# Kernel tuning notes

Hardware: AMD Instinct MI355X
Metric: run time of the kernel (lower is better)

The kernel has to match this reference:

```python
import jax, jax.numpy as jnp
import numpy as np

D_MODEL = 2048
NUM_HEADS = 16
HEAD_DIM = D_MODEL // NUM_HEADS  # 128; scale uses head_dim even though attention is over full d_model
B, S = 2, 2048


def setup_inputs() -> dict:
    key = jax.random.key(0)
    ks = jax.random.split(key, 5)
    x = jax.random.normal(ks[0], (B, S, D_MODEL), dtype=jnp.float32)
    # causal additive mask, as typically passed to this module (2D, sliced mask[-s:, :kv])
    neg = jnp.float32(-1e9)
    mask = jnp.where(jnp.triu(jnp.ones((S, S), dtype=bool), k=1), neg, jnp.float32(0.0))
    std = 1.0 / np.sqrt(D_MODEL)
    Wq = jax.random.normal(ks[1], (D_MODEL, D_MODEL), dtype=jnp.float32) * std
    Wk = jax.random.normal(ks[2], (D_MODEL, D_MODEL), dtype=jnp.float32) * std
    Wv = jax.random.normal(ks[3], (D_MODEL, D_MODEL), dtype=jnp.float32) * std
    Wo = jax.random.normal(ks[4], (D_MODEL, D_MODEL), dtype=jnp.float32) * std
    return {"x": x, "mask": mask, "Wq": Wq, "Wk": Wk, "Wv": Wv, "Wo": Wo}


def reference(x, mask, Wq, Wk, Wv, Wo):
    # nn.Linear(bias=False): y = x @ W^T
    q = jnp.einsum('bsd,ed->bse', x, Wq)  # [B,S,D]
    k = jnp.einsum('bsd,ed->bse', x, Wk)
    v = jnp.einsum('bsd,ed->bse', x, Wv)
    scale = jnp.float32(HEAD_DIM ** -0.5)
    # NOTE: faithful to source — contraction over full d_model, no head split
    scores = jnp.einsum('bsd,btd->bst', q, k) * scale  # [B,S,S]
    scores = scores + mask  # mask[-s:, :kv] == mask here (s == kv)
    weights = jax.nn.softmax(scores, axis=-1)
    out = jnp.einsum('bst,btd->bsd', weights, v)
    return jnp.einsum('bsd,ed->bse', out, Wo)
```

## Files before the change

### kernel.cpp

```cpp
#include <hip/hip_runtime.h>

#define DM  2048
#define SQ  2048
#define NB  2
#define BSZ (NB * SQ)

typedef _Float16 f16x8 __attribute__((ext_vector_type(8)));
typedef __attribute__((ext_vector_type(4))) float f32x4;

#define ASG(p) (const __attribute__((address_space(1))) void*)(p)
#define ASL(p) (__attribute__((address_space(3))) void*)(p)

__device__ __forceinline__ unsigned short f2h(float f) {
  union { _Float16 h; unsigned short u; } x;
  x.h = (_Float16)f;
  return x.u;
}

__global__ __launch_bounds__(256) void cast_f32(const float4* __restrict__ in,
                                                ushort4* __restrict__ out,
                                                int n4) {
  int i = blockIdx.x * 256 + threadIdx.x;
  if (i >= n4) return;
  float4 v = in[i];
  ushort4 h;
  h.x = f2h(v.x); h.y = f2h(v.y); h.z = f2h(v.z); h.w = f2h(v.w);
  out[i] = h;
}

__global__ __launch_bounds__(256) void cast_w4(const float4* __restrict__ a,
                                               const float4* __restrict__ b,
                                               const float4* __restrict__ c,
                                               const float4* __restrict__ d,
                                               ushort4* __restrict__ out,
                                               int n4per) {
  int i = blockIdx.x * 256 + threadIdx.x;
  int seg = i / n4per, j = i - seg * n4per;
  const float4* src = (seg == 0) ? a : (seg == 1) ? b : (seg == 2) ? c : d;
  float4 v = src[j];
  ushort4 h;
  h.x = f2h(v.x); h.y = f2h(v.y); h.z = f2h(v.z); h.w = f2h(v.w);
  out[i] = h;
}

#define SB() __builtin_amdgcn_sched_barrier(0)
#define BARX() do { SB(); __builtin_amdgcn_s_barrier(); SB(); } while (0)

#define STAGE8(BUFL, HALF, T) do { \
    const unsigned short* G_ = ((HALF) < 2) ? Ab : Bb; \
    const int ldG_ = ((HALF) < 2) ? ldA : ldB; \
    const int r0_ = (((HALF) < 2) ? bm0 : bn0) + ((HALF) & 1) * 128; \
    const long k0_ = (long)((T) << 6); \
    char* db_ = ldsb + (BUFL) * 65536 + (HALF) * 16384 + tid * 16; \
    const unsigned short* s0_ = G_ + (long)(r0_ + srow) * ldG_ + k0_ + scsw; \
    const unsigned short* s1_ = G_ + (long)(r0_ + 64 + srow) * ldG_ + k0_ + scsw; \
    __builtin_amdgcn_global_load_lds(ASG(s0_), ASL(db_), 16, 0, 0); \
    __builtin_amdgcn_global_load_lds(ASG(s1_), ASL(db_ + 8192), 16, 0, 0); \
  } while (0)

#define LDA8(BUFL, MQ, Af) do { \
    const char* ba_ = ldsb + (BUFL) * 65536 + wm * 16384 + (MQ) * 8192 + arow; \
    _Pragma("unroll") for (int mm_ = 0; mm_ < 4; mm_++) { \
      Af[mm_][0] = *(const f16x8*)(ba_ + mm_ * 2048 + sl0); \
      Af[mm_][1] = *(const f16x8*)(ba_ + mm_ * 2048 + sl1); } \
  } while (0)

#define LDB8(BUFL, NQ, Bf) do { \
    const char* bb_ = ldsb + (BUFL) * 65536 + 32768 + (wn * 2 + (NQ)) * 4096 + arow; \
    _Pragma("unroll") for (int nn_ = 0; nn_ < 2; nn_++) { \
      Bf[nn_][0] = *(const f16x8*)(bb_ + nn_ * 2048 + sl0); \
      Bf[nn_][1] = *(const f16x8*)(bb_ + nn_ * 2048 + sl1); } \
  } while (0)

#define PH8(Af, Bf, MQ, NQ) do { \
    __builtin_amdgcn_s_setprio(1); \
    _Pragma("unroll") for (int ks_ = 0; ks_ < 2; ks_++) \
    _Pragma("unroll") for (int mm_ = 0; mm_ < 4; mm_++) \
    _Pragma("unroll") for (int nn_ = 0; nn_ < 2; nn_++) \
      acc[(MQ) * 4 + mm_][(NQ) * 2 + nn_] = __builtin_amdgcn_mfma_f32_16x16x32_f16( \
          Af[mm_][ks_], Bf[nn_][ks_], acc[(MQ) * 4 + mm_][(NQ) * 2 + nn_], 0, 0, 0); \
    __builtin_amdgcn_s_setprio(0); \
  } while (0)

#define GROUP8(BUFL, T) do { \
    LDA8(BUFL, 0, a0); LDB8(BUFL, 0, b0); \
    LDA8(BUFL, 1, a1); \
    if ((T) + 1 < NT) STAGE8(BUFL ^ 1, 3, (T) + 1); \
    PH8(a0, b0, 0, 0); \
    BARX(); \
    LDB8(BUFL, 1, b1); \
    PH8(a1, b0, 1, 0); \
    BARX(); \
    if ((T) + 2 < NT) STAGE8(BUFL, 0, (T) + 2); \
    PH8(a1, b1, 1, 1); \
    BARX(); \
    if ((T) + 2 < NT) { STAGE8(BUFL, 1, (T) + 2); STAGE8(BUFL, 2, (T) + 2); } \
    PH8(a0, b1, 0, 1); \
    SB(); \
    if ((T) + 1 < NT) { \
      if ((T) + 1 == NT - 1) { asm volatile("s_waitcnt vmcnt(0)" ::: "memory"); } \
      else                   { asm volatile("s_waitcnt vmcnt(6)" ::: "memory"); } \
    } \
    __builtin_amdgcn_s_barrier(); \
    SB(); \
  } while (0)

template <int OM>
__global__ __launch_bounds__(512, 2) void gemm8p(
    const unsigned short* __restrict__ A, const unsigned short* __restrict__ B,
    float* __restrict__ Cf, unsigned short* __restrict__ Ch,
    int K, int ldA, int ldB, int ldC) {
  __shared__ __align__(16) char ldsarr[131072];
  char* ldsb = ldsarr;

  const int bm0 = blockIdx.x * 256;
  const int bn0 = blockIdx.y * 256;
  const unsigned short* Ab = A;
  const unsigned short* Bb = B;

  const int tid = threadIdx.x, lane = tid & 63, wid = tid >> 6;
  const int wm = wid >> 2, wn = wid & 3;
  const int fr = lane & 15, fq = lane >> 4;
  const int NT = K >> 6;

  const int sl0 = ((fq ^ (fr & 7)) << 4);
  const int sl1 = (((4 + fq) ^ (fr & 7)) << 4);
  const int arow = fr << 7;

  const int srow = tid >> 3;
  const int scsw = ((tid & 7) ^ (srow & 7)) << 3;

  f32x4 acc[8][4];
#pragma unroll
  for (int m = 0; m < 8; m++)
#pragma unroll
    for (int n = 0; n < 4; n++)
#pragma unroll
      for (int r = 0; r < 4; r++) acc[m][n][r] = 0.f;

  f16x8 a0[4][2], a1[4][2], b0[2][2], b1[2][2];

  STAGE8(0, 0, 0); STAGE8(0, 1, 0); STAGE8(0, 2, 0); STAGE8(0, 3, 0);
  STAGE8(1, 0, 1); STAGE8(1, 1, 1); STAGE8(1, 2, 1);
  asm volatile("s_waitcnt vmcnt(6)" ::: "memory");
  __builtin_amdgcn_s_barrier();
  SB();

  for (int t = 0; t < NT; t += 2) {
    GROUP8(0, t);
    GROUP8(1, t + 1);
  }

#pragma unroll
  for (int mq = 0; mq < 2; mq++)
#pragma unroll
    for (int mm = 0; mm < 4; mm++)
#pragma unroll
      for (int nq = 0; nq < 2; nq++)
#pragma unroll
        for (int nn = 0; nn < 2; nn++) {
          const int col = bn0 + wn * 64 + nq * 32 + nn * 16 + fr;
#pragma unroll
          for (int r = 0; r < 4; r++) {
            const long row = (long)bm0 + wm * 128 + mq * 64 + mm * 16 + fq * 4 + r;
            const long ci = row * ldC + col;
            if constexpr (OM == 0) Cf[ci] = acc[mq * 4 + mm][nq * 2 + nn][r];
            else                   Ch[ci] = f2h(acc[mq * 4 + mm][nq * 2 + nn][r]);
          }
        }
}

#define STAGER(BUFL, REG, U, T) do { \
    const unsigned short* G_ = (REG) ? Bb : Ab; \
    const int ldG_ = (REG) ? ldB : ldA; \
    const int r0_ = ((REG) ? bn0 : bm0) + (U) * 64; \
    const long k0_ = (long)((T) << 6); \
    char* db_ = ldsb + (BUFL) * 49152 + (REG) * 16384 + (U) * 8192 + tid * 16; \
    const unsigned short* s_ = G_ + (long)(r0_ + srow) * ldG_ + k0_ + scsw; \
    __builtin_amdgcn_global_load_lds(ASG(s_), ASL(db_), 16, 0, 0); \
  } while (0)

#define LDAR(BUFL, MH, Af) do { \
    const char* ba_ = ldsb + (BUFL) * 49152 + (wm * 64 + (MH) * 32) * 128 + arow; \
    _Pragma("unroll") for (int mm_ = 0; mm_ < 2; mm_++) { \
      Af[mm_][0] = *(const f16x8*)(ba_ + mm_ * 2048 + sl0); \
      Af[mm_][1] = *(const f16x8*)(ba_ + mm_ * 2048 + sl1); } \
  } while (0)

#define LDBR(BUFL, NH, Bf) do { \
    const char* bb_ = ldsb + (BUFL) * 49152 + 16384 + (wn * 64 + (NH) * 32) * 128 + arow; \
    _Pragma("unroll") for (int nn_ = 0; nn_ < 2; nn_++) { \
      Bf[nn_][0] = *(const f16x8*)(bb_ + nn_ * 2048 + sl0); \
      Bf[nn_][1] = *(const f16x8*)(bb_ + nn_ * 2048 + sl1); } \
  } while (0)

#define PHR(Af, Bf, MH, NH) do { \
    __builtin_amdgcn_s_setprio(1); \
    _Pragma("unroll") for (int ks_ = 0; ks_ < 2; ks_++) \
    _Pragma("unroll") for (int mm_ = 0; mm_ < 2; mm_++) \
    _Pragma("unroll") for (int nn_ = 0; nn_ < 2; nn_++) \
      acc[(MH) * 2 + mm_][(NH) * 2 + nn_] = __builtin_amdgcn_mfma_f32_16x16x32_f16( \
          Af[mm_][ks_], Bf[nn_][ks_], acc[(MH) * 2 + mm_][(NH) * 2 + nn_], 0, 0, 0); \
    __builtin_amdgcn_s_setprio(0); \
  } while (0)

#define GROUPR(BUFL, T) do { \
    LDAR(BUFL, 0, a0); LDBR(BUFL, 0, b0); \
    LDAR(BUFL, 1, a1); \
    if ((T) + 1 < NT) STAGER(BUFL ^ 1, 1, 3, (T) + 1); \
    PHR(a0, b0, 0, 0); \
    BARX(); \
    LDBR(BUFL, 1, b1); \
    PHR(a1, b0, 1, 0); \
    BARX(); \
    if ((T) + 2 < NT) { STAGER(BUFL, 0, 0, (T) + 2); STAGER(BUFL, 0, 1, (T) + 2); } \
    PHR(a1, b1, 1, 1); \
    BARX(); \
    if ((T) + 2 < NT) { STAGER(BUFL, 1, 0, (T) + 2); STAGER(BUFL, 1, 1, (T) + 2); STAGER(BUFL, 1, 2, (T) + 2); } \
    PHR(a0, b1, 0, 1); \
    SB(); \
    if ((T) + 1 < NT) { \
      if ((T) + 1 == NT - 1) { asm volatile("s_waitcnt vmcnt(0)" ::: "memory"); } \
      else                   { asm volatile("s_waitcnt vmcnt(5)" ::: "memory"); } \
    } \
    __builtin_amdgcn_s_barrier(); \
    SB(); \
  } while (0)

template <int OM, int CAUSAL>
__global__ __launch_bounds__(512, 2) void gemm8pR(
    const unsigned short* __restrict__ A, const unsigned short* __restrict__ B,
    float* __restrict__ Cf, unsigned short* __restrict__ Ch,
    int K, long sAb, long sBb, long sCb,
    int ldA, int ldB, int ldC, float alpha) {
  __shared__ __align__(16) char ldsarr[98304];
  char* ldsb = ldsarr;

  const int bm0 = blockIdx.x * 128;
  const int bn0 = blockIdx.y * 256;
  if (CAUSAL == 1 && bn0 > bm0 + 127) return;

  const int z = blockIdx.z;
  const unsigned short* Ab = A + (long)z * sAb;
  const unsigned short* Bb = B + (long)z * sBb;
  const long cb = (long)z * sCb;

  const int tid = threadIdx.x, lane = tid & 63, wid = tid >> 6;
  const int wm = wid >> 2, wn = wid & 3;
  const int fr = lane & 15, fq = lane >> 4;
  int NT = K >> 6;
  if (CAUSAL == 2) NT = (bm0 + 128) >> 6;

  const int sl0 = ((fq ^ (fr & 7)) << 4);
  const int sl1 = (((4 + fq) ^ (fr & 7)) << 4);
  const int arow = fr << 7;

  const int srow = tid >> 3;
  const int scsw = ((tid & 7) ^ (srow & 7)) << 3;

  f32x4 acc[4][4];
#pragma unroll
  for (int m = 0; m < 4; m++)
#pragma unroll
    for (int n = 0; n < 4; n++)
#pragma unroll
      for (int r = 0; r < 4; r++) acc[m][n][r] = 0.f;

  f16x8 a0[2][2], a1[2][2], b0[2][2], b1[2][2];

  STAGER(0, 0, 0, 0); STAGER(0, 0, 1, 0);
  STAGER(0, 1, 0, 0); STAGER(0, 1, 1, 0); STAGER(0, 1, 2, 0); STAGER(0, 1, 3, 0);
  STAGER(1, 0, 0, 1); STAGER(1, 0, 1, 1);
  STAGER(1, 1, 0, 1); STAGER(1, 1, 1, 1); STAGER(1, 1, 2, 1);
  asm volatile("s_waitcnt vmcnt(5)" ::: "memory");
  __builtin_amdgcn_s_barrier();
  SB();

  for (int t = 0; t < NT; t += 2) {
    GROUPR(0, t);
    GROUPR(1, t + 1);
  }

#pragma unroll
  for (int mh = 0; mh < 2; mh++)
#pragma unroll
    for (int mm = 0; mm < 2; mm++)
#pragma unroll
      for (int nh = 0; nh < 2; nh++)
#pragma unroll
        for (int nn = 0; nn < 2; nn++) {
          const int col = bn0 + wn * 64 + nh * 32 + nn * 16 + fr;
#pragma unroll
          for (int r = 0; r < 4; r++) {
            const long row = (long)bm0 + wm * 64 + mh * 32 + mm * 16 + fq * 4 + r;
            const long ci = cb + row * ldC + col;
            const float vv = acc[mh * 2 + mm][nh * 2 + nn][r] * alpha;
            if constexpr (OM == 0) Cf[ci] = vv;
            else                   Ch[ci] = f2h(vv);
          }
        }
}

__global__ __launch_bounds__(256) void softmax_causal(const float* __restrict__ sc,
                                                      unsigned short* __restrict__ pr) {
  const int row = blockIdx.x;
  const int s = row & (SQ - 1);
  const long base = (long)row * SQ;
  const int n = s + 1;
  const int tid = threadIdx.x;
  const int lane = tid & 63;
  const int wv = tid >> 6;
  __shared__ float red[4];

  float v[8];
  float mx = -3.0e38f;
#pragma unroll
  for (int j = 0; j < 8; j++) {
    const int i = tid + j * 256;
    v[j] = (i < n) ? sc[base + i] : -3.0e38f;
    mx = fmaxf(mx, v[j]);
  }
#pragma unroll
  for (int o = 32; o >= 1; o >>= 1) mx = fmaxf(mx, __shfl_xor(mx, o));
  if (lane == 0) red[wv] = mx;
  __syncthreads();
  mx = fmaxf(fmaxf(red[0], red[1]), fmaxf(red[2], red[3]));
  __syncthreads();

  float sum = 0.f;
#pragma unroll
  for (int j = 0; j < 8; j++) {
    const int i = tid + j * 256;
    v[j] = (i < n) ? __expf(v[j] - mx) : 0.f;
    sum += v[j];
  }
#pragma unroll
  for (int o = 32; o >= 1; o >>= 1) sum += __shfl_xor(sum, o);
  if (lane == 0) red[wv] = sum;
  __syncthreads();
  const float inv = 1.f / (red[0] + red[1] + red[2] + red[3]);
#pragma unroll
  for (int j = 0; j < 8; j++) {
    const int i = tid + j * 256;
    pr[base + i] = (i < n) ? f2h(v[j] * inv) : (unsigned short)0;
  }
}

extern "C" void kernel_launch(void* const* d_in, const int* in_sizes, int n_in,
                              void* d_out, int out_size, void* d_ws, size_t ws_size,
                              hipStream_t stream) {
  (void)in_sizes; (void)n_in; (void)out_size; (void)ws_size;
  const float* x  = (const float*)d_in[0];
  const float* Wq = (const float*)d_in[2];
  const float* Wk = (const float*)d_in[3];
  const float* Wv = (const float*)d_in[4];
  const float* Wo = (const float*)d_in[5];
  float* out = (float*)d_out;

  const long ELx = (long)BSZ * DM;
  const long ELw = (long)DM * DM;

  char* ws = (char*)d_ws;
  size_t off = 0;
  auto take = [&](size_t bytes) { void* p = ws + off; off += bytes; return p; };

  unsigned short* x16   = (unsigned short*)take(ELx * 2);
  unsigned short* wqk16 = (unsigned short*)take(2 * ELw * 2);
  unsigned short* wv16  = (unsigned short*)take(ELw * 2);
  unsigned short* wo16  = (unsigned short*)take(ELw * 2);
  unsigned short* qk16  = (unsigned short*)take((long)BSZ * 2 * DM * 2);
  unsigned short* vTT   = (unsigned short*)take(ELx * 2);
  unsigned short* probs = (unsigned short*)take((long)NB * SQ * SQ * 2);
  float* scores = (float*)ws;
  unsigned short* ctx = qk16;
  unsigned short* q16 = qk16;
  unsigned short* k16 = qk16 + DM;

  const int n4x = (int)(ELx / 4), n4w = (int)(ELw / 4);
  cast_f32<<<dim3(n4x / 256), 256, 0, stream>>>((const float4*)x, (ushort4*)x16, n4x);
  cast_w4<<<dim3(4 * n4w / 256), 256, 0, stream>>>(
      (const float4*)Wq, (const float4*)Wk, (const float4*)Wv, (const float4*)Wo,
      (ushort4*)wqk16, n4w);

  const float scale = 0.08838834764831845f;

  gemm8p<1><<<dim3(BSZ / 256, 2 * DM / 256), 512, 0, stream>>>(
      x16, wqk16, nullptr, qk16, DM, DM, DM, 2 * DM);
  gemm8pR<1, 0><<<dim3(DM / 128, BSZ / 256, 1), 512, 0, stream>>>(
      wv16, x16, nullptr, vTT, DM, 0L, 0L, 0L, DM, DM, BSZ, 1.0f);
  gemm8pR<0, 1><<<dim3(SQ / 128, SQ / 256, NB), 512, 0, stream>>>(
      q16, k16, scores, nullptr, DM, (long)SQ * 2 * DM, (long)SQ * 2 * DM,
      (long)SQ * SQ, 2 * DM, 2 * DM, SQ, scale);

  softmax_causal<<<dim3(NB * SQ), 256, 0, stream>>>(scores, probs);

  gemm8pR<1, 2><<<dim3(SQ / 128, DM / 256, NB), 512, 0, stream>>>(
      probs, vTT, nullptr, ctx, SQ, (long)SQ * SQ, 2048L, (long)SQ * DM,
      SQ, BSZ, DM, 1.0f);
  gemm8pR<0, 0><<<dim3(BSZ / 128, DM / 256, 1), 512, 0, stream>>>(
      ctx, wo16, out, nullptr, DM, 0L, 0L, 0L, DM, DM, DM, 1.0f);
}
```

Baseline: 251.8 us.

## Store attention scores in fp16, vectorize softmax, merge cast kernels

The QK^T GEMM now writes scores as fp16 into the reused x16 workspace instead of fp32, which halves score write and read traffic. Softmax reads and writes 8 contiguous fp16 values per thread with 128-bit accesses. The two cast kernels are merged into one launch, and the MFMA loop order is changed so the k-steps for the same accumulator are adjacent. Storing scores in fp16 loses precision and could overflow for large logits, and reusing x16 is safe only because x16 is no longer read after the V projection.

After: 240.3 us. 1.05x faster.

```diff
diff --git a/kernel.cpp b/kernel.cpp
--- a/kernel.cpp
+++ b/kernel.cpp
@@ -16,28 +16,30 @@
   x.h = (_Float16)f;
   return x.u;
 }
-
-__global__ __launch_bounds__(256) void cast_f32(const float4* __restrict__ in,
+__device__ __forceinline__ float h2f(unsigned short u) {
+  union { unsigned short u; _Float16 h; } x;
+  x.u = u;
+  return (float)x.h;
+}
+
+__global__ __launch_bounds__(256) void cast_all(const float4* __restrict__ x,
+                                                const float4* __restrict__ wq,
+                                                const float4* __restrict__ wk,
+                                                const float4* __restrict__ wv,
+                                                const float4* __restrict__ wo,
                                                 ushort4* __restrict__ out,
-                                                int n4) {
+                                                int n4x, int n4w) {
   int i = blockIdx.x * 256 + threadIdx.x;
-  if (i >= n4) return;
-  float4 v = in[i];
-  ushort4 h;
-  h.x = f2h(v.x); h.y = f2h(v.y); h.z = f2h(v.z); h.w = f2h(v.w);
-  out[i] = h;
-}
-
-__global__ __launch_bounds__(256) void cast_w4(const float4* __restrict__ a,
-                                               const float4* __restrict__ b,
-                                               const float4* __restrict__ c,
-                                               const float4* __restrict__ d,
-                                               ushort4* __restrict__ out,
-                                               int n4per) {
-  int i = blockIdx.x * 256 + threadIdx.x;
-  int seg = i / n4per, j = i - seg * n4per;
-  const float4* src = (seg == 0) ? a : (seg == 1) ? b : (seg == 2) ? c : d;
-  float4 v = src[j];
+  float4 v;
+  if (i < n4x) {
+    v = x[i];
+  } else {
+    int j = i - n4x;
+    int seg = j >> 20;
+    int off = j & (n4w - 1);
+    const float4* src = (seg == 0) ? wq : (seg == 1) ? wk : (seg == 2) ? wv : wo;
+    v = src[off];
+  }
   ushort4 h;
   h.x = f2h(v.x); h.y = f2h(v.y); h.z = f2h(v.z); h.w = f2h(v.w);
   out[i] = h;
@@ -74,9 +76,9 @@
 
 #define PH8(Af, Bf, MQ, NQ) do { \
     __builtin_amdgcn_s_setprio(1); \
-    _Pragma("unroll") for (int ks_ = 0; ks_ < 2; ks_++) \
     _Pragma("unroll") for (int mm_ = 0; mm_ < 4; mm_++) \
     _Pragma("unroll") for (int nn_ = 0; nn_ < 2; nn_++) \
+    _Pragma("unroll") for (int ks_ = 0; ks_ < 2; ks_++) \
       acc[(MQ) * 4 + mm_][(NQ) * 2 + nn_] = __builtin_amdgcn_mfma_f32_16x16x32_f16( \
           Af[mm_][ks_], Bf[nn_][ks_], acc[(MQ) * 4 + mm_][(NQ) * 2 + nn_], 0, 0, 0); \
     __builtin_amdgcn_s_setprio(0); \
@@ -196,9 +198,9 @@
 
 #define PHR(Af, Bf, MH, NH) do { \
     __builtin_amdgcn_s_setprio(1); \
-    _Pragma("unroll") for (int ks_ = 0; ks_ < 2; ks_++) \
     _Pragma("unroll") for (int mm_ = 0; mm_ < 2; mm_++) \
     _Pragma("unroll") for (int nn_ = 0; nn_ < 2; nn_++) \
+    _Pragma("unroll") for (int ks_ = 0; ks_ < 2; ks_++) \
       acc[(MH) * 2 + mm_][(NH) * 2 + nn_] = __builtin_amdgcn_mfma_f32_16x16x32_f16( \
           Af[mm_][ks_], Bf[nn_][ks_], acc[(MH) * 2 + mm_][(NH) * 2 + nn_], 0, 0, 0); \
     __builtin_amdgcn_s_setprio(0); \
@@ -301,7 +303,7 @@
         }
 }
 
-__global__ __launch_bounds__(256) void softmax_causal(const float* __restrict__ sc,
+__global__ __launch_bounds__(256) void softmax_causal(const unsigned short* __restrict__ sc,
                                                       unsigned short* __restrict__ pr) {
   const int row = blockIdx.x;
   const int s = row & (SQ - 1);
@@ -310,14 +312,17 @@
   const int tid = threadIdx.x;
   const int lane = tid & 63;
   const int wv = tid >> 6;
+  const int e0 = tid * 8;
   __shared__ float red[4];
+
+  union { uint4 u4; unsigned short us[8]; } in, ou;
+  in.u4 = *(const uint4*)&sc[base + e0];
 
   float v[8];
   float mx = -3.0e38f;
 #pragma unroll
   for (int j = 0; j < 8; j++) {
-    const int i = tid + j * 256;
-    v[j] = (i < n) ? sc[base + i] : -3.0e38f;
+    v[j] = (e0 + j < n) ? h2f(in.us[j]) : -3.0e38f;
     mx = fmaxf(mx, v[j]);
   }
 #pragma unroll
@@ -330,8 +335,7 @@
   float sum = 0.f;
 #pragma unroll
   for (int j = 0; j < 8; j++) {
-    const int i = tid + j * 256;
-    v[j] = (i < n) ? __expf(v[j] - mx) : 0.f;
+    v[j] = (e0 + j < n) ? __expf(v[j] - mx) : 0.f;
     sum += v[j];
   }
 #pragma unroll
@@ -340,10 +344,8 @@
   __syncthreads();
   const float inv = 1.f / (red[0] + red[1] + red[2] + red[3]);
 #pragma unroll
-  for (int j = 0; j < 8; j++) {
-    const int i = tid + j * 256;
-    pr[base + i] = (i < n) ? f2h(v[j] * inv) : (unsigned short)0;
-  }
+  for (int j = 0; j < 8; j++) ou.us[j] = (e0 + j < n) ? f2h(v[j] * inv) : (unsigned short)0;
+  *(uint4*)&pr[base + e0] = ou.u4;
 }
 
 extern "C" void kernel_launch(void* const* d_in, const int* in_sizes, int n_in,
@@ -371,16 +373,15 @@
   unsigned short* qk16  = (unsigned short*)take((long)BSZ * 2 * DM * 2);
   unsigned short* vTT   = (unsigned short*)take(ELx * 2);
   unsigned short* probs = (unsigned short*)take((long)NB * SQ * SQ * 2);
-  float* scores = (float*)ws;
+  unsigned short* scores = x16;
   unsigned short* ctx = qk16;
   unsigned short* q16 = qk16;
   unsigned short* k16 = qk16 + DM;
 
   const int n4x = (int)(ELx / 4), n4w = (int)(ELw / 4);
-  cast_f32<<<dim3(n4x / 256), 256, 0, stream>>>((const float4*)x, (ushort4*)x16, n4x);
-  cast_w4<<<dim3(4 * n4w / 256), 256, 0, stream>>>(
-      (const float4*)Wq, (const float4*)Wk, (const float4*)Wv, (const float4*)Wo,
-      (ushort4*)wqk16, n4w);
+  cast_all<<<dim3((n4x + 4 * n4w) / 256), 256, 0, stream>>>(
+      (const float4*)x, (const float4*)Wq, (const float4*)Wk,
+      (const float4*)Wv, (const float4*)Wo, (ushort4*)x16, n4x, n4w);
 
   const float scale = 0.08838834764831845f;
 
@@ -388,8 +389,8 @@
       x16, wqk16, nullptr, qk16, DM, DM, DM, 2 * DM);
   gemm8pR<1, 0><<<dim3(DM / 128, BSZ / 256, 1), 512, 0, stream>>>(
       wv16, x16, nullptr, vTT, DM, 0L, 0L, 0L, DM, DM, BSZ, 1.0f);
-  gemm8pR<0, 1><<<dim3(SQ / 128, SQ / 256, NB), 512, 0, stream>>>(
-      q16, k16, scores, nullptr, DM, (long)SQ * 2 * DM, (long)SQ * 2 * DM,
+  gemm8pR<1, 1><<<dim3(SQ / 128, SQ / 256, NB), 512, 0, stream>>>(
+      q16, k16, nullptr, scores, DM, (long)SQ * 2 * DM, (long)SQ * 2 * DM,
       (long)SQ * SQ, 2 * DM, 2 * DM, SQ, scale);
 
   softmax_causal<<<dim3(NB * SQ), 256, 0, stream>>>(scores, probs);
```
